# Kernel tuning notes

Measured on AMD Instinct MI355X. Metric: run time of the kernel, lower is better.

Reference implementation:

```python
import jax, jax.numpy as jnp
import numpy as np

B, S, C, H = 8, 1024, 512, 8
DH = C // H  # channels per head


def setup_inputs() -> dict:
    key = jax.random.key(0)
    ks = jax.random.split(key, 10)
    s = 1.0 / np.sqrt(C)
    return {
        "pe_lin_encoding": jax.random.normal(ks[0], (B, S, C), jnp.float32),
        "pe_lin_skip": jax.random.normal(ks[1], (B, S, C), jnp.float32),
        "Wq": jax.random.normal(ks[2], (C, C), jnp.float32) * s,
        "bq": jax.random.normal(ks[3], (C,), jnp.float32) * s,
        "Wk": jax.random.normal(ks[4], (C, C), jnp.float32) * s,
        "bk": jax.random.normal(ks[5], (C,), jnp.float32) * s,
        "Wv": jax.random.normal(ks[6], (C, C), jnp.float32) * s,
        "bv": jax.random.normal(ks[7], (C,), jnp.float32) * s,
        "Wo": jax.random.normal(ks[8], (C, C), jnp.float32) * s,
        "bo": jax.random.normal(ks[9], (C,), jnp.float32) * s,
    }


def reference(pe_lin_encoding, pe_lin_skip, Wq, bq, Wk, bk, Wv, bv, Wo, bo):
    # flatten trailing dims (already [B, S, C] here)
    x = pe_lin_encoding.reshape(pe_lin_encoding.shape[0], pe_lin_encoding.shape[1], -1)
    # torch Linear convention: y = x @ W^T + b, W is [out, in]
    q = jnp.einsum("bsc,oc->bso", x, Wq) + bq
    k = jnp.einsum("bsc,oc->bso", x, Wk) + bk
    v = jnp.einsum("bsc,oc->bso", x, Wv) + bv
    # split heads: [B, S, H, DH] -> attention per head
    q = q.reshape(B, S, H, DH)
    k = k.reshape(B, S, H, DH)
    v = v.reshape(B, S, H, DH)
    scale = 1.0 / np.sqrt(DH)
    scores = jnp.einsum("bqhd,bkhd->bhqk", q, k) * scale  # [B,H,S,S]
    attn = jax.nn.softmax(scores, axis=-1)
    ctx = jnp.einsum("bhqk,bkhd->bqhd", attn, v).reshape(B, S, C)
    out = jnp.einsum("bsc,oc->bso", ctx, Wo) + bo
    return out + pe_lin_skip
```

## Files before the change

kernel.cpp:

```cpp
#include <hip/hip_runtime.h>
#include <hip/hip_bf16.h>

typedef unsigned short u16;
typedef unsigned int u32;

constexpr int B  = 8;
constexpr int S  = 1024;
constexpr int C  = 512;
constexpr int H  = 8;
constexpr int DH = 64;
constexpr int M  = B * S;

typedef __attribute__((ext_vector_type(8))) short bf16x8;
typedef __attribute__((ext_vector_type(4))) float f32x4;
typedef __attribute__((ext_vector_type(16))) float f32x16;
typedef __attribute__((ext_vector_type(4))) u32 u32x4;

#define GLOBAL_AS __attribute__((address_space(1)))
#define LDS_AS    __attribute__((address_space(3)))

#define QSCALE 0.1803368867f

__device__ __forceinline__ float bf2f(u16 u) {
    return __uint_as_float(((u32)u) << 16);
}
__device__ __forceinline__ u16 f2bf(float f) {
    u32 u = __float_as_uint(f);
    u += 0x7fffu + ((u >> 16) & 1u);
    return (u16)(u >> 16);
}
__device__ __forceinline__ u32 pack2(float a, float b) {
    return (u32)f2bf(a) | ((u32)f2bf(b) << 16);
}
__device__ __forceinline__ u32 cvtpk(float a, float b) {
    u32 d;
    asm("v_cvt_pk_bf16_f32 %0, %1, %2" : "=v"(d) : "v"(a), "v"(b));
    return d;
}
__device__ __forceinline__ void async_cp16(const u16* g, u16* l) {
    __builtin_amdgcn_global_load_lds((const GLOBAL_AS void*)g, (LDS_AS void*)l, 16, 0, 0);
}
__device__ __forceinline__ f32x16 zero16() {
    f32x16 z;
    #pragma unroll
    for (int i = 0; i < 16; i++) z[i] = 0.f;
    return z;
}

constexpr int NX4 = M * C / 4;
constexpr int NW4 = C * C / 4;

__global__ __launch_bounds__(256) void cvt_kernel(
    const float* __restrict__ x,
    const float* __restrict__ wq, const float* __restrict__ wk,
    const float* __restrict__ wv, const float* __restrict__ wo,
    u16* __restrict__ xb, u16* __restrict__ wqkv, u16* __restrict__ wob)
{
    const int i = blockIdx.x * 256 + threadIdx.x;
    const float* src; u16* dst; int off;
    if      (i < NX4)          { src = x;  dst = xb;           off = i; }
    else if (i < NX4 +   NW4)  { src = wq; dst = wqkv;         off = i - NX4; }
    else if (i < NX4 + 2*NW4)  { src = wk; dst = wqkv + C*C;   off = i - NX4 -   NW4; }
    else if (i < NX4 + 3*NW4)  { src = wv; dst = wqkv + 2*C*C; off = i - NX4 - 2*NW4; }
    else                       { src = wo; dst = wob;          off = i - NX4 - 3*NW4; }
    float4 v = ((const float4*)src)[off];
    uint2 p; p.x = pack2(v.x, v.y); p.y = pack2(v.z, v.w);
    ((uint2*)dst)[off] = p;
}

__global__ __launch_bounds__(256) void qkv_gemm(
    const u16* __restrict__ xb, const u16* __restrict__ wqkv,
    const float* __restrict__ bq, const float* __restrict__ bk,
    const float* __restrict__ bv,
    u16* __restrict__ Qo, u16* __restrict__ Ko, u16* __restrict__ Vo)
{
    __shared__ alignas(16) u16 smem[128 * 136];
    u16* const Asm = smem;
    u16* const Bsm = smem + 128 * 64;

    const int mTile = blockIdx.x * 128;
    const int nTile = blockIdx.y * 128;
    const int t = threadIdx.x, lane = t & 63, w = t >> 6;
    const int ql = lane & 15, quad = lane >> 4;
    const int wm = (w & 1) * 64, wn = (w >> 1) * 64;

    f32x4 acc[4][4];
    #pragma unroll
    for (int i = 0; i < 4; i++)
        #pragma unroll
        for (int j = 0; j < 4; j++) acc[i][j] = (f32x4){0.f, 0.f, 0.f, 0.f};

    for (int k0 = 0; k0 < C; k0 += 64) {
        __syncthreads();
        #pragma unroll
        for (int q = 0; q < 4; q++) {
            const int chunk = q * 256 + t;
            const int row = chunk >> 3, c8 = (chunk & 7) * 8;
            async_cp16(xb   + (size_t)(mTile + row) * C + k0 + c8, &Asm[row * 64 + c8]);
            async_cp16(wqkv + (size_t)(nTile + row) * C + k0 + c8, &Bsm[row * 64 + c8]);
        }
        __syncthreads();

        #pragma unroll
        for (int ks = 0; ks < 64; ks += 32) {
            bf16x8 af[4], bfr[4];
            #pragma unroll
            for (int i = 0; i < 4; i++)
                af[i] = *(const bf16x8*)&Asm[(wm + i*16 + ql) * 64 + ks + quad*8];
            #pragma unroll
            for (int j = 0; j < 4; j++)
                bfr[j] = *(const bf16x8*)&Bsm[(wn + j*16 + ql) * 64 + ks + quad*8];
            #pragma unroll
            for (int i = 0; i < 4; i++)
                #pragma unroll
                for (int j = 0; j < 4; j++)
                    acc[i][j] = __builtin_amdgcn_mfma_f32_16x16x32_bf16(af[i], bfr[j], acc[i][j], 0, 0, 0);
        }
    }

    const int z = nTile >> 9;
    const int nBase = nTile & 511;
    if (z == 2) {
        __syncthreads();
        u16* const T = smem;
        #pragma unroll
        for (int j = 0; j < 4; j++) {
            const int n = wn + j*16 + ql;
            const float bj = bv[nBase + n];
            #pragma unroll
            for (int i = 0; i < 4; i++)
                #pragma unroll
                for (int r = 0; r < 4; r++)
                    T[n * 136 + wm + i*16 + quad*4 + r] = f2bf(acc[i][j][r] + bj);
        }
        __syncthreads();
        const int bb = mTile >> 10, ssBase = mTile & 1023;
        #pragma unroll
        for (int q = 0; q < 8; q++) {
            const int c = q * 256 + t;
            const int row = c >> 4, col = (c & 15) * 8;
            const int o = nBase + row, h = o >> 6, d = o & 63;
            *(float4*)(Vo + ((size_t)((bb*H + h) * DH + d)) * S + ssBase + col) =
                *(const float4*)&T[row * 136 + col];
        }
    } else {
        const float* bias = (z == 0) ? bq : bk;
        u16* dst          = (z == 0) ? Qo : Ko;
        const float sc    = (z == 0) ? QSCALE : 1.0f;
        #pragma unroll
        for (int j = 0; j < 4; j++) {
            const int o = nBase + wn + j*16 + ql;
            const float bj = bias[o];
            const int h = o >> 6, d = o & 63;
            #pragma unroll
            for (int i = 0; i < 4; i++) {
                #pragma unroll
                for (int r = 0; r < 4; r++) {
                    const int m = mTile + wm + i*16 + quad*4 + r;
                    const int bb = m >> 10, ss = m & 1023;
                    dst[(size_t)((bb*H + h) * S + ss) * DH + d] = f2bf((acc[i][j][r] + bj) * sc);
                }
            }
        }
    }
}

__global__ __launch_bounds__(256) void attn_kernel(
    const u16* __restrict__ Qo,
    const u16* __restrict__ Ko,
    const u16* __restrict__ Vo,
    u16* __restrict__ ctx)
{
    __shared__ alignas(16) u16 KVs[2][2][2][64 * 64];

    const int g = blockIdx.x;
    const int xcd = g & 7, slot = g >> 3;
    const int bh = xcd * 8 + (slot >> 4);
    const int qt = slot & 15;

    const int t = threadIdx.x;
    const int lane = t & 63, w = t >> 6;
    const int qg = w & 1, kg = w >> 1;
    const int l31 = lane & 31, hi = lane >> 5;
    const int sxh8 = ((l31 & 7) ^ hi) << 3;
    const int kRow = l31 * 64;

    const u16* __restrict__ Qb = Qo + (size_t)bh * S * DH;
    const u16* __restrict__ Kb = Ko + (size_t)bh * S * DH;
    const u16* __restrict__ Vt = Vo + (size_t)bh * DH * S;

    const int qrow = qt * 64 + qg * 32 + l31;
    bf16x8 qf[4];
    #pragma unroll
    for (int ks = 0; ks < 4; ks++)
        qf[ks] = *(const bf16x8*)(Qb + (size_t)qrow * DH + ks * 16 + hi * 8);

    f32x16 acc[2];
    acc[0] = zero16(); acc[1] = zero16();
    float dsum = 0.f;

    const int tp = t & 127;
    const int kBase = kg * 512;

    auto STAGE = [&](int buf, int it) {
        const int k0 = kBase + it * 64;
        u16* const Kd = &KVs[buf][kg][0][0];
        u16* const Vd = &KVs[buf][kg][1][0];
        #pragma unroll
        for (int q = 0; q < 4; ++q) {
            const int gi = q * 128 + tp;
            const int row = gi >> 3, cc = gi & 7;
            const int c = cc ^ (row & 7);
            async_cp16(Kb + (size_t)(k0 + row) * DH + c * 8, &Kd[gi * 8]);
            async_cp16(Vt + (size_t)row * S + k0 + c * 8,    &Vd[gi * 8]);
        }
    };

    STAGE(0, 0);
    #pragma unroll 2
    for (int it = 0; it < 8; ++it) {
        const int cur = it & 1;
        if (it + 1 < 8) {
            STAGE(cur ^ 1, it + 1);
            asm volatile("s_waitcnt vmcnt(8)" ::: "memory");
        } else {
            asm volatile("s_waitcnt vmcnt(0)" ::: "memory");
        }
        asm volatile("s_barrier" ::: "memory");

        const u16* const Kh = &KVs[cur][kg][0][0];
        const u16* const Vh = &KVs[cur][kg][1][0];

        #pragma unroll
        for (int kt = 0; kt < 2; ++kt) {
            f32x16 sc = zero16();
            #pragma unroll
            for (int ks = 0; ks < 4; ++ks) {
                const bf16x8 kf = *(const bf16x8*)&Kh[kRow + kt * 2048 + ((ks << 4) ^ sxh8)];
                sc = __builtin_amdgcn_mfma_f32_32x32x16_bf16(kf, qf[ks], sc, 0, 0, 0);
            }
            #pragma unroll
            for (int s = 0; s < 2; ++s) {
                float e0 = exp2f(sc[8*s+0]), e1 = exp2f(sc[8*s+1]);
                float e2 = exp2f(sc[8*s+2]), e3 = exp2f(sc[8*s+3]);
                float e4 = exp2f(sc[8*s+4]), e5 = exp2f(sc[8*s+5]);
                float e6 = exp2f(sc[8*s+6]), e7 = exp2f(sc[8*s+7]);
                dsum += ((e0 + e1) + (e2 + e3)) + ((e4 + e5) + (e6 + e7));
                u32 x0 = cvtpk(e0, e1), x1 = cvtpk(e2, e3);
                u32 y0 = cvtpk(e4, e5), y1 = cvtpk(e6, e7);
                asm("v_permlane32_swap_b32 %0, %1" : "+v"(x0), "+v"(y0));
                asm("v_permlane32_swap_b32 %0, %1" : "+v"(x1), "+v"(y1));
                u32x4 pw; pw.x = x0; pw.y = x1; pw.z = y0; pw.w = y1;
                const bf16x8 pa = __builtin_bit_cast(bf16x8, pw);

                const int ccol = (((kt * 4 + s * 2) << 3) ^ sxh8);
                acc[0] = __builtin_amdgcn_mfma_f32_32x32x16_bf16(
                    pa, *(const bf16x8*)&Vh[kRow + ccol], acc[0], 0, 0, 0);
                acc[1] = __builtin_amdgcn_mfma_f32_32x32x16_bf16(
                    pa, *(const bf16x8*)&Vh[kRow + 2048 + ccol], acc[1], 0, 0, 0);
            }
        }
        asm volatile("s_barrier" ::: "memory");
    }

    float dtot = dsum + __shfl_xor(dsum, 32);

    __syncthreads();
    float* F = (float*)&KVs[0][0][0][0];
    if (kg == 1) {
        #pragma unroll
        for (int r = 0; r < 16; ++r) F[r * 128 + qg * 64 + lane] = acc[0][r];
        #pragma unroll
        for (int r = 0; r < 16; ++r) F[(16 + r) * 128 + qg * 64 + lane] = acc[1][r];
        F[32 * 128 + qg * 64 + lane] = dtot;
    }
    __syncthreads();
    if (kg == 0) {
        #pragma unroll
        for (int r = 0; r < 16; ++r) acc[0][r] += F[r * 128 + qg * 64 + lane];
        #pragma unroll
        for (int r = 0; r < 16; ++r) acc[1][r] += F[(16 + r) * 128 + qg * 64 + lane];
        dtot += F[32 * 128 + qg * 64 + lane];

        const int b_ = bh >> 3, h = bh & 7;
        const int qbase2 = qt * 64 + qg * 32 + 4 * hi;
        #pragma unroll
        for (int r = 0; r < 16; ++r) {
            const int cr = (r & 3) + 8 * (r >> 2);
            const float dr = __shfl(dtot, 4 * hi + cr);
            const float inv = 1.0f / dr;
            const int srow = qbase2 + cr;
            const size_t base = ((size_t)(b_ * S + srow)) * C + h * DH + l31;
            ctx[base]      = f2bf(acc[0][r] * inv);
            ctx[base + 32] = f2bf(acc[1][r] * inv);
        }
    }
}

__global__ __launch_bounds__(256) void out_gemm(
    const u16* __restrict__ ctx, const u16* __restrict__ wob,
    const float* __restrict__ bo, const float* __restrict__ skip,
    float* __restrict__ out)
{
    __shared__ alignas(16) u16 Asm[128 * 64];
    __shared__ alignas(16) u16 Bsm[128 * 64];

    const int mTile = blockIdx.x * 128;
    const int nTile = blockIdx.y * 128;
    const int t = threadIdx.x, lane = t & 63, w = t >> 6;
    const int ql = lane & 15, quad = lane >> 4;
    const int wm = (w & 1) * 64, wn = (w >> 1) * 64;

    f32x4 acc[4][4];
    #pragma unroll
    for (int i = 0; i < 4; i++)
        #pragma unroll
        for (int j = 0; j < 4; j++) acc[i][j] = (f32x4){0.f, 0.f, 0.f, 0.f};

    for (int k0 = 0; k0 < C; k0 += 64) {
        __syncthreads();
        #pragma unroll
        for (int q = 0; q < 4; q++) {
            const int chunk = q * 256 + t;
            const int row = chunk >> 3, c8 = (chunk & 7) * 8;
            async_cp16(ctx + (size_t)(mTile + row) * C + k0 + c8, &Asm[row * 64 + c8]);
            async_cp16(wob + (size_t)(nTile + row) * C + k0 + c8, &Bsm[row * 64 + c8]);
        }
        __syncthreads();

        #pragma unroll
        for (int ks = 0; ks < 64; ks += 32) {
            bf16x8 af[4], bfr[4];
            #pragma unroll
            for (int i = 0; i < 4; i++)
                af[i] = *(const bf16x8*)&Asm[(wm + i*16 + ql) * 64 + ks + quad*8];
            #pragma unroll
            for (int j = 0; j < 4; j++)
                bfr[j] = *(const bf16x8*)&Bsm[(wn + j*16 + ql) * 64 + ks + quad*8];
            #pragma unroll
            for (int i = 0; i < 4; i++)
                #pragma unroll
                for (int j = 0; j < 4; j++)
                    acc[i][j] = __builtin_amdgcn_mfma_f32_16x16x32_bf16(af[i], bfr[j], acc[i][j], 0, 0, 0);
        }
    }

    #pragma unroll
    for (int j = 0; j < 4; j++) {
        const int o = nTile + wn + j*16 + ql;
        const float bj = bo[o];
        #pragma unroll
        for (int i = 0; i < 4; i++) {
            #pragma unroll
            for (int r = 0; r < 4; r++) {
                const int m = mTile + wm + i*16 + quad*4 + r;
                const size_t idx = (size_t)m * C + o;
                out[idx] = acc[i][j][r] + bj + skip[idx];
            }
        }
    }
}

extern "C" void kernel_launch(void* const* d_in, const int* in_sizes, int n_in,
                              void* d_out, int out_size, void* d_ws, size_t ws_size,
                              hipStream_t stream) {
    (void)in_sizes; (void)n_in; (void)out_size; (void)ws_size;
    const float* x    = (const float*)d_in[0];
    const float* skip = (const float*)d_in[1];
    const float* Wq   = (const float*)d_in[2];
    const float* bq   = (const float*)d_in[3];
    const float* Wk   = (const float*)d_in[4];
    const float* bk   = (const float*)d_in[5];
    const float* Wv   = (const float*)d_in[6];
    const float* bv   = (const float*)d_in[7];
    const float* Wo   = (const float*)d_in[8];
    const float* bo   = (const float*)d_in[9];
    float* out = (float*)d_out;

    u16* xb   = (u16*)d_ws;
    u16* wqkv = xb   + (size_t)M * C;
    u16* wob  = wqkv + (size_t)3 * C * C;
    u16* Qo   = wob  + (size_t)C * C;
    u16* Ko   = Qo   + (size_t)B * H * S * DH;
    u16* Vo   = Ko   + (size_t)B * H * S * DH;
    u16* ctx  = xb;

    cvt_kernel<<<dim3((NX4 + 4 * NW4) / 256), 256, 0, stream>>>(
        x, Wq, Wk, Wv, Wo, xb, wqkv, wob);
    qkv_gemm<<<dim3(M / 128, 1536 / 128), 256, 0, stream>>>(
        xb, wqkv, bq, bk, bv, Qo, Ko, Vo);
    attn_kernel<<<dim3(1024), 256, 0, stream>>>(Qo, Ko, Vo, ctx);
    out_gemm<<<dim3(M / 128, C / 128), 256, 0, stream>>>(
        ctx, wob, bo, skip, out);
}
```

Before: 175.0 us.

## Stage GEMM epilogues through LDS for coalesced stores; prioritize attention MFMAs

```diff
diff --git a/kernel.cpp b/kernel.cpp
--- a/kernel.cpp
+++ b/kernel.cpp
@@ -120,6 +120,7 @@
 
     const int z = nTile >> 9;
     const int nBase = nTile & 511;
+    const int bb = mTile >> 10, ssBase = mTile & 1023;
     if (z == 2) {
         __syncthreads();
         u16* const T = smem;
@@ -134,7 +135,6 @@
                     T[n * 136 + wm + i*16 + quad*4 + r] = f2bf(acc[i][j][r] + bj);
         }
         __syncthreads();
-        const int bb = mTile >> 10, ssBase = mTile & 1023;
         #pragma unroll
         for (int q = 0; q < 8; q++) {
             const int c = q * 256 + t;
@@ -147,20 +147,26 @@
         const float* bias = (z == 0) ? bq : bk;
         u16* dst          = (z == 0) ? Qo : Ko;
         const float sc    = (z == 0) ? QSCALE : 1.0f;
+        __syncthreads();
+        u16* const T = smem;
         #pragma unroll
         for (int j = 0; j < 4; j++) {
-            const int o = nBase + wn + j*16 + ql;
-            const float bj = bias[o];
-            const int h = o >> 6, d = o & 63;
-            #pragma unroll
-            for (int i = 0; i < 4; i++) {
+            const int n = wn + j*16 + ql;
+            const float bj = bias[nBase + n];
+            #pragma unroll
+            for (int i = 0; i < 4; i++)
                 #pragma unroll
-                for (int r = 0; r < 4; r++) {
-                    const int m = mTile + wm + i*16 + quad*4 + r;
-                    const int bb = m >> 10, ss = m & 1023;
-                    dst[(size_t)((bb*H + h) * S + ss) * DH + d] = f2bf((acc[i][j][r] + bj) * sc);
-                }
-            }
+                for (int r = 0; r < 4; r++)
+                    T[(wm + i*16 + quad*4 + r) * 136 + n] = f2bf((acc[i][j][r] + bj) * sc);
+        }
+        __syncthreads();
+        #pragma unroll
+        for (int q = 0; q < 8; q++) {
+            const int c = q * 256 + t;
+            const int row = c >> 4, col = (c & 15) * 8;
+            const int o = nBase + col, h = o >> 6, d = o & 63;
+            *(float4*)(dst + ((size_t)((bb*H + h) * S + (ssBase + row))) * DH + d) =
+                *(const float4*)&T[row * 136 + col];
         }
     }
 }
@@ -234,11 +240,13 @@
         #pragma unroll
         for (int kt = 0; kt < 2; ++kt) {
             f32x16 sc = zero16();
+            __builtin_amdgcn_s_setprio(1);
             #pragma unroll
             for (int ks = 0; ks < 4; ++ks) {
                 const bf16x8 kf = *(const bf16x8*)&Kh[kRow + kt * 2048 + ((ks << 4) ^ sxh8)];
                 sc = __builtin_amdgcn_mfma_f32_32x32x16_bf16(kf, qf[ks], sc, 0, 0, 0);
             }
+            __builtin_amdgcn_s_setprio(0);
             #pragma unroll
             for (int s = 0; s < 2; ++s) {
                 float e0 = exp2f(sc[8*s+0]), e1 = exp2f(sc[8*s+1]);
@@ -254,10 +262,12 @@
                 const bf16x8 pa = __builtin_bit_cast(bf16x8, pw);
 
                 const int ccol = (((kt * 4 + s * 2) << 3) ^ sxh8);
+                __builtin_amdgcn_s_setprio(1);
                 acc[0] = __builtin_amdgcn_mfma_f32_32x32x16_bf16(
                     pa, *(const bf16x8*)&Vh[kRow + ccol], acc[0], 0, 0, 0);
                 acc[1] = __builtin_amdgcn_mfma_f32_32x32x16_bf16(
                     pa, *(const bf16x8*)&Vh[kRow + 2048 + ccol], acc[1], 0, 0, 0);
+                __builtin_amdgcn_s_setprio(0);
             }
         }
         asm volatile("s_barrier" ::: "memory");
@@ -302,8 +312,9 @@
     const float* __restrict__ bo, const float* __restrict__ skip,
     float* __restrict__ out)
 {
-    __shared__ alignas(16) u16 Asm[128 * 64];
-    __shared__ alignas(16) u16 Bsm[128 * 64];
+    __shared__ alignas(16) u16 smem[128 * 132];
+    u16* const Asm = smem;
+    u16* const Bsm = smem + 128 * 64;
 
     const int mTile = blockIdx.x * 128;
     const int nTile = blockIdx.y * 128;
@@ -345,18 +356,34 @@
         }
     }
 
+    float* const F2 = (float*)smem;
     #pragma unroll
-    for (int j = 0; j < 4; j++) {
-        const int o = nTile + wn + j*16 + ql;
-        const float bj = bo[o];
-        #pragma unroll
-        for (int i = 0; i < 4; i++) {
-            #pragma unroll
-            for (int r = 0; r < 4; r++) {
-                const int m = mTile + wm + i*16 + quad*4 + r;
-                const size_t idx = (size_t)m * C + o;
-                out[idx] = acc[i][j][r] + bj + skip[idx];
+    for (int p = 0; p < 2; ++p) {
+        __syncthreads();
+        if ((w >> 1) == p) {
+            #pragma unroll
+            for (int j = 0; j < 4; j++) {
+                const int n = j*16 + ql;
+                #pragma unroll
+                for (int i = 0; i < 4; i++)
+                    #pragma unroll
+                    for (int r = 0; r < 4; r++)
+                        F2[(wm + i*16 + quad*4 + r) * 66 + n] = acc[i][j][r];
             }
+        }
+        __syncthreads();
+        #pragma unroll
+        for (int q8 = 0; q8 < 8; ++q8) {
+            const int c = q8 * 256 + t;
+            const int row = c >> 4, col4 = (c & 15) * 4;
+            const int m = mTile + row, o = nTile + p*64 + col4;
+            const float4 v  = *(const float4*)&F2[row * 66 + col4];
+            const float4 s4 = *(const float4*)&skip[(size_t)m * C + o];
+            const float4 b4 = *(const float4*)&bo[o];
+            float4 r4;
+            r4.x = v.x + b4.x + s4.x;  r4.y = v.y + b4.y + s4.y;
+            r4.z = v.z + b4.z + s4.z;  r4.w = v.w + b4.w + s4.w;
+            *(float4*)&out[(size_t)m * C + o] = r4;
         }
     }
 }
```

Result: no change. 175.6 us (+0.4%).
